# Optimization experiments

Hardware: AMD Instinct MI355X
Metric: run time of the kernel (lower is better)

The kernel has to match this reference:

```python
import jax, jax.numpy as jnp
import numpy as np

N_NODES = 100000
N_EDGES = 1600000
K = 3  # TAGConv default hops


def _make_lin(key, out_dim, in_dim):
    # K+1 bias-free linears (stacked) + one shared output bias, per PyG TAGConv
    kw, = jax.random.split(key, 1)
    scale = 1.0 / np.sqrt(in_dim)
    W = jax.random.uniform(kw, (K + 1, out_dim, in_dim), jnp.float32, -scale, scale)
    b = jnp.zeros((out_dim,), jnp.float32)
    return W, b


def setup_inputs() -> dict:
    key = jax.random.key(0)
    ks = jax.random.split(key, 6)
    x = jax.random.normal(ks[0], (N_NODES, 128), jnp.float32)
    edge_index = jax.random.randint(ks[1], (2, N_EDGES), 0, N_NODES, jnp.int64)
    W1, b1 = _make_lin(ks[2], 128, 128)
    W2, b2 = _make_lin(ks[3], 64, 128)
    W3, b3 = _make_lin(ks[4], 16, 64)
    return {"x": x, "edge_index": edge_index, "W1": W1, "b1": b1,
            "W2": W2, "b2": b2, "W3": W3, "b3": b3}


def _tagconv(x, row, col, norm, W, b, n):
    # out = sum_k lin_k(A_norm^k x) + b ; message x_j*norm gathered at col
    out = jnp.einsum('nd,od->no', x, W[0])
    h = x
    for k in range(1, W.shape[0]):
        h = jax.ops.segment_sum(norm[:, None] * h[row], col, num_segments=n)
        out = out + jnp.einsum('nd,od->no', h, W[k])
    return out + b


def _dropout(x, key, p=0.5):
    keep = jax.random.bernoulli(key, 1.0 - p, x.shape)
    return jnp.where(keep, x / (1.0 - p), 0.0)


def reference(x, edge_index, W1, b1, W2, b2, W3, b3):
    n = x.shape[0]
    row, col = edge_index[0], edge_index[1]
    # gcn_norm without self-loops (TAGConv default)
    deg = jax.ops.segment_sum(jnp.ones(row.shape[0], x.dtype), col, num_segments=n)
    dis = jnp.where(deg > 0, 1.0 / jnp.sqrt(jnp.where(deg > 0, deg, 1.0)), 0.0)
    norm = dis[row] * dis[col]

    dk1, dk2 = jax.random.split(jax.random.key(42))
    h = _tagconv(x, row, col, norm, W1, b1, n)
    h = _dropout(h, dk1)
    h = _tagconv(h, row, col, norm, W2, b2, n)
    h = jax.nn.elu(h)
    h = _dropout(h, dk2)
    h = _tagconv(h, row, col, norm, W3, b3, n)
    return h
```

## Files before the change

### kernel.cpp

```cpp
#include <hip/hip_runtime.h>
#include <stdint.h>
#include <math.h>

#define N_NODES 100000
#define N_EDGES 1600000

typedef __bf16 bf16_t;
typedef __attribute__((ext_vector_type(4))) __bf16 bf16x4;
typedef __attribute__((ext_vector_type(8))) __bf16 bf16x8;
typedef __attribute__((ext_vector_type(4))) float f32x4;

__device__ __forceinline__ f32x4 mfma16(bf16x8 a, bf16x8 b, f32x4 c) {
  return __builtin_amdgcn_mfma_f32_16x16x32_bf16(a, b, c, 0, 0, 0);
}

__device__ __host__ __forceinline__ uint32_t rotl32(uint32_t v, int d) {
  return (v << d) | (v >> (32 - d));
}

__device__ __host__ __forceinline__ void threefry2x32(uint32_t k0, uint32_t k1,
                                                      uint32_t x0, uint32_t x1,
                                                      uint32_t& o0, uint32_t& o1) {
  uint32_t ks0 = k0, ks1 = k1, ks2 = k0 ^ k1 ^ 0x1BD11BDAu;
  x0 += ks0; x1 += ks1;
#define TF_R(r) { x0 += x1; x1 = rotl32(x1, r); x1 ^= x0; }
  TF_R(13) TF_R(15) TF_R(26) TF_R(6)
  x0 += ks1; x1 += ks2 + 1u;
  TF_R(17) TF_R(29) TF_R(16) TF_R(24)
  x0 += ks2; x1 += ks0 + 2u;
  TF_R(13) TF_R(15) TF_R(26) TF_R(6)
  x0 += ks0; x1 += ks1 + 3u;
  TF_R(17) TF_R(29) TF_R(16) TF_R(24)
  x0 += ks1; x1 += ks2 + 4u;
  TF_R(13) TF_R(15) TF_R(26) TF_R(6)
  x0 += ks2; x1 += ks0 + 5u;
#undef TF_R
  o0 = x0; o1 = x1;
}

__device__ __forceinline__ float drop_scale(uint32_t idx, uint32_t k0, uint32_t k1) {
  uint32_t o0, o1;
  threefry2x32(k0, k1, 0u, idx, o0, o1);
  uint32_t bits = o0 ^ o1;
  float u = __uint_as_float((bits >> 9) | 0x3f800000u) - 1.0f;
  return (u < 0.5f) ? 2.0f : 0.0f;
}

__global__ __launch_bounds__(256) void detect_kernel(const int* __restrict__ ei,
                                                     int* __restrict__ found_nonzero) {
  int idx = blockIdx.x * 256 + threadIdx.x;
  size_t j = (size_t)idx * 781;
  if (ei[2 * j + 1] != 0) atomicOr(found_nonzero, 1);
}

__device__ __forceinline__ int edge_row(const int* ei, bool i32, int e) {
  return i32 ? ei[e] : ei[2 * (size_t)e];
}
__device__ __forceinline__ int edge_col(const int* ei, bool i32, int e) {
  return i32 ? ei[N_EDGES + e] : ei[2 * ((size_t)N_EDGES + (size_t)e)];
}

#define BKT_SHIFT 8
#define NBKT 391
#define BKT_CAP 6144
#define EPB 8192
#define NBLK 196
#define SCAN_M (NBKT * NBLK)

__global__ __launch_bounds__(256) void hist_kernel(const int* __restrict__ ei,
                                                   const int* __restrict__ flag,
                                                   int* __restrict__ hist) {
  __shared__ int h[NBKT];
  const int t = threadIdx.x, blk = blockIdx.x;
  for (int i = t; i < NBKT; i += 256) h[i] = 0;
  __syncthreads();
  const bool i32 = *flag != 0;
  const int e0 = blk * EPB;
  for (int i = t; i < EPB; i += 256) {
    int e = e0 + i;
    if (e < N_EDGES) atomicAdd(&h[edge_col(ei, i32, e) >> BKT_SHIFT], 1);
  }
  __syncthreads();
  for (int i = t; i < NBKT; i += 256) hist[i * NBLK + blk] = h[i];
}

__global__ __launch_bounds__(256) void btot_kernel(const int* __restrict__ hist,
                                                   int* __restrict__ btot) {
  __shared__ int sh[256];
  const int b = blockIdx.x, t = threadIdx.x;
  int s = 0;
  for (int i = t; i < NBLK; i += 256) s += hist[b * NBLK + i];
  sh[t] = s;
  __syncthreads();
  for (int ofs = 128; ofs > 0; ofs >>= 1) {
    if (t < ofs) sh[t] += sh[t + ofs];
    __syncthreads();
  }
  if (t == 0) btot[b] = sh[0];
}

__global__ __launch_bounds__(512) void bbase_kernel(const int* __restrict__ btot,
                                                    int* __restrict__ bbase,
                                                    int* __restrict__ S) {
  __shared__ int sh[512];
  const int t = threadIdx.x;
  int v = (t < NBKT) ? btot[t] : 0;
  sh[t] = v;
  __syncthreads();
  for (int ofs = 1; ofs < 512; ofs <<= 1) {
    int u = (t >= ofs) ? sh[t - ofs] : 0;
    __syncthreads();
    sh[t] += u;
    __syncthreads();
  }
  if (t < NBKT) bbase[t] = sh[t] - v;
  if (t == 0) S[SCAN_M] = N_EDGES;
}

__global__ __launch_bounds__(256) void bscan2_kernel(const int* __restrict__ hist,
                                                     const int* __restrict__ bbase,
                                                     int* __restrict__ S) {
  __shared__ int sh[256];
  const int b = blockIdx.x, t = threadIdx.x;
  int v = (t < NBLK) ? hist[b * NBLK + t] : 0;
  sh[t] = v;
  __syncthreads();
  for (int ofs = 1; ofs < 256; ofs <<= 1) {
    int u = (t >= ofs) ? sh[t - ofs] : 0;
    __syncthreads();
    sh[t] += u;
    __syncthreads();
  }
  if (t < NBLK) S[b * NBLK + t] = bbase[b] + sh[t] - v;
}

__global__ __launch_bounds__(256) void binfill_kernel(const int* __restrict__ ei,
                                                      const int* __restrict__ flag,
                                                      const int* __restrict__ S,
                                                      int2* __restrict__ bins) {
  __shared__ int cur[NBKT];
  const int t = threadIdx.x, blk = blockIdx.x;
  for (int i = t; i < NBKT; i += 256) cur[i] = S[i * NBLK + blk];
  __syncthreads();
  const bool i32 = *flag != 0;
  const int e0 = blk * EPB;
  for (int i = t; i < EPB; i += 256) {
    int e = e0 + i;
    if (e < N_EDGES) {
      int r = edge_row(ei, i32, e);
      int c = edge_col(ei, i32, e);
      int p = atomicAdd(&cur[c >> BKT_SHIFT], 1);
      bins[p] = make_int2(r, c);
    }
  }
}

__global__ __launch_bounds__(512) void degdis_scatter_kernel(
    const int2* __restrict__ bins, const int* __restrict__ S,
    float* __restrict__ dis, int* __restrict__ rptr,
    uint32_t* __restrict__ erow) {
  __shared__ int h[256];
  __shared__ int sc[256];
  __shared__ int loff[256];
  __shared__ int lcur[256];
  __shared__ uint32_t reord[BKT_CAP];
  const int b = blockIdx.x, t = threadIdx.x;
  const int Bb = S[b * NBLK];
  const int Be = S[(b + 1) * NBLK];
  const int cnt = min(Be - Bb, BKT_CAP);
  if (t < 256) h[t] = 0;
  __syncthreads();
  for (int i = t; i < cnt; i += 512)
    atomicAdd(&h[bins[Bb + i].y & 255], 1);
  __syncthreads();
  if (t < 256) sc[t] = h[t];
  __syncthreads();
  for (int ofs = 1; ofs < 256; ofs <<= 1) {
    int u = 0;
    if (t >= ofs && t < 256) u = sc[t - ofs];
    __syncthreads();
    if (t < 256) sc[t] += u;
    __syncthreads();
  }
  const int c0 = b << BKT_SHIFT;
  const int nn = min(256, N_NODES - c0);
  if (t < 256) {
    loff[t] = sc[t] - h[t];
    lcur[t] = 0;
    if (t < nn) {
      int d = h[t];
      dis[c0 + t] = (d > 0) ? (1.0f / sqrtf((float)d)) : 0.0f;
      rptr[c0 + t] = Bb + sc[t] - d;
    }
  }
  if (b == NBKT - 1 && t == 0) rptr[N_NODES] = N_EDGES;
  __syncthreads();
  for (int i = t; i < cnt; i += 512) {
    int2 rec = bins[Bb + i];
    int lc = rec.y & 255;
    int p = atomicAdd(&lcur[lc], 1);
    reord[loff[lc] + p] = (uint32_t)rec.x;
  }
  __syncthreads();
  for (int i = t; i < cnt; i += 512) erow[Bb + i] = reord[i];
}

__global__ __launch_bounds__(256) void wcvt_kernel(
    const float* __restrict__ W1, const float* __restrict__ W2,
    const float* __restrict__ W3,
    bf16_t* __restrict__ Wb1, bf16_t* __restrict__ Wb2,
    bf16_t* __restrict__ Wb3) {
  int i = blockIdx.x * 256 + threadIdx.x;
  if (i < 65536) Wb1[i] = (bf16_t)W1[i];
  if (i < 32768) Wb2[i] = (bf16_t)W2[i];
  if (i < 4096)  Wb3[i] = (bf16_t)W3[i];
}

template <int DIN, int LOG_DOUT, int NCH, bool YB, bool AHL>
__global__ __launch_bounds__(256) void matmul_mfma_kernel(
    const void* __restrict__ hA, const void* __restrict__ hAlo,
    const bf16_t* __restrict__ Wb, const float* __restrict__ bias,
    float* __restrict__ y0, void* __restrict__ y1,
    void* __restrict__ y2, void* __restrict__ y3) {
  constexpr int LDK = DIN + 8;
  constexpr int DOUT = 1 << LOG_DOUT;
  constexpr int KI = DIN / 32;
  __shared__ bf16_t sm[2][64 * LDK];
  const int m0 = blockIdx.x * 64;
  const int tid = threadIdx.x;

  if (AHL) {
    constexpr int NL = 64 * DIN / 8 / 256;
#pragma unroll
    for (int it = 0; it < NL; ++it) {
      int idx = tid + it * 256;
      int r = idx / (DIN / 8), cc = (idx % (DIN / 8)) * 8;
      int gm = m0 + r;
      uint4 vh = make_uint4(0, 0, 0, 0), vl = make_uint4(0, 0, 0, 0);
      if (gm < N_NODES) {
        vh = ((const uint4*)hA)[((size_t)gm * DIN + cc) >> 3];
        vl = ((const uint4*)hAlo)[((size_t)gm * DIN + cc) >> 3];
      }
      *(uint4*)&sm[0][r * LDK + cc] = vh;
      *(uint4*)&sm[1][r * LDK + cc] = vl;
    }
  } else {
    constexpr int NL = 64 * DIN / 4 / 256;
    union U4 { bf16_t b[4]; uint2 u; };
#pragma unroll
    for (int it = 0; it < NL; ++it) {
      int idx = tid + it * 256;
      int r = idx / (DIN / 4), cc = (idx % (DIN / 4)) * 4;
      int gm = m0 + r;
      float4 v = (gm < N_NODES) ? ((const float4*)hA)[((size_t)gm * DIN + cc) >> 2]
                                : make_float4(0.f, 0.f, 0.f, 0.f);
      U4 hi, lo;
      hi.b[0] = (bf16_t)v.x; lo.b[0] = (bf16_t)(v.x - (float)hi.b[0]);
      hi.b[1] = (bf16_t)v.y; lo.b[1] = (bf16_t)(v.y - (float)hi.b[1]);
      hi.b[2] = (bf16_t)v.z; lo.b[2] = (bf16_t)(v.z - (float)hi.b[2]);
      hi.b[3] = (bf16_t)v.w; lo.b[3] = (bf16_t)(v.w - (float)hi.b[3]);
      *(uint2*)&sm[0][r * LDK + cc] = hi.u;
      *(uint2*)&sm[1][r * LDK + cc] = lo.u;
    }
  }
  __syncthreads();

  const int w = tid >> 6, lane = tid & 63;
  const int wm = w & 1, wn = w >> 1;
  const int quad = lane >> 4, lr = lane & 15;

  bf16x8 aH[2][KI], aL[2][KI];
#pragma unroll
  for (int mt = 0; mt < 2; ++mt)
#pragma unroll
    for (int ki = 0; ki < KI; ++ki) {
      int rowa = wm * 32 + mt * 16 + lr;
      int koff = ki * 32 + quad * 8;
      aH[mt][ki] = *(const bf16x8*)&sm[0][rowa * LDK + koff];
      aL[mt][ki] = *(const bf16x8*)&sm[1][rowa * LDK + koff];
    }
  __syncthreads();

  constexpr int NLB = 64 * DIN / 8 / 256;
  uint4 wreg[NLB];
#pragma unroll
  for (int it = 0; it < NLB; ++it) {
    int idx = tid + it * 256;
    int r = idx / (DIN / 8), cc = (idx % (DIN / 8)) * 8;
    wreg[it] = ((const uint4*)Wb)[(((size_t)r) * DIN + cc) >> 3];
    *(uint4*)&sm[0][r * LDK + cc] = wreg[it];
  }
  __syncthreads();

  for (int nc = 0; nc < NCH; ++nc) {
    int p = nc & 1;
    if (nc + 1 < NCH) {
#pragma unroll
      for (int it = 0; it < NLB; ++it) {
        int idx = tid + it * 256;
        int r = idx / (DIN / 8), cc = (idx % (DIN / 8)) * 8;
        wreg[it] = ((const uint4*)Wb)[(((size_t)((nc + 1) * 64 + r)) * DIN + cc) >> 3];
      }
    }

    f32x4 acc[2][2] = {};
#pragma unroll
    for (int ki = 0; ki < KI; ++ki) {
      int koff = ki * 32 + quad * 8;
      bf16x8 bfr[2];
#pragma unroll
      for (int nt = 0; nt < 2; ++nt)
        bfr[nt] = *(const bf16x8*)&sm[p][(wn * 32 + nt * 16 + lr) * LDK + koff];
#pragma unroll
      for (int mt = 0; mt < 2; ++mt)
#pragma unroll
        for (int nt = 0; nt < 2; ++nt) {
          acc[mt][nt] = mfma16(bfr[nt], aH[mt][ki], acc[mt][nt]);
          acc[mt][nt] = mfma16(bfr[nt], aL[mt][ki], acc[mt][nt]);
        }
    }

    if (nc + 1 < NCH) {
#pragma unroll
      for (int it = 0; it < NLB; ++it) {
        int idx = tid + it * 256;
        int r = idx / (DIN / 8), cc = (idx % (DIN / 8)) * 8;
        *(uint4*)&sm[p ^ 1][r * LDK + cc] = wreg[it];
      }
    }
    __syncthreads();

    const int n0 = nc * 64;
#pragma unroll
    for (int mt = 0; mt < 2; ++mt) {
      int m = m0 + wm * 32 + mt * 16 + lr;
      if (m >= N_NODES) continue;
#pragma unroll
      for (int nt = 0; nt < 2; ++nt) {
        int nb = n0 + wn * 32 + nt * 16 + quad * 4;
        int k = nb >> LOG_DOUT;
        int o = nb & (DOUT - 1);
        size_t oi = (size_t)m * DOUT + o;
        if (k == 0) {
          float4 bv = *(const float4*)&bias[o];
          float4 st = make_float4(acc[mt][nt][0] + bv.x, acc[mt][nt][1] + bv.y,
                                  acc[mt][nt][2] + bv.z, acc[mt][nt][3] + bv.w);
          *(float4*)&y0[oi] = st;
        } else {
          void* yk = (k == 1) ? y1 : (k == 2) ? y2 : y3;
          if (YB) {
            bf16x4 bb;
            bb.x = (bf16_t)acc[mt][nt][0];
            bb.y = (bf16_t)acc[mt][nt][1];
            bb.z = (bf16_t)acc[mt][nt][2];
            bb.w = (bf16_t)acc[mt][nt][3];
            *(bf16x4*)((bf16_t*)yk + oi) = bb;
          } else {
            *(f32x4*)((float*)yk + oi) = acc[mt][nt];
          }
        }
      }
    }
  }
}

template <int D, int EPI, bool ABF, int OMODE>
__global__ __launch_bounds__(256) void prop_kernel(
    const bf16_t* __restrict__ zv, const void* __restrict__ addv,
    void* __restrict__ outv, void* __restrict__ outv2,
    const int* __restrict__ rptr, const uint32_t* __restrict__ erow,
    const float* __restrict__ dis, uint32_t k0, uint32_t k1) {
  constexpr int LPN = D / 4;
  constexpr int NPB = 256 / LPN;
  const int lane = threadIdx.x % LPN;
  const int nsub = threadIdx.x / LPN;
  const int c = blockIdx.x * NPB + nsub;
  if (c >= N_NODES) return;
  const int e0 = rptr[c], e1 = rptr[c + 1];
  const float dc = dis[c];
  const bf16x4* zs = (const bf16x4*)zv;
  float a0 = 0.f, a1 = 0.f, a2 = 0.f, a3 = 0.f;

  int e = e0;
  for (; e + 7 < e1; e += 8) {
    uint32_t r8[8];
#pragma unroll
    for (int j = 0; j < 8; ++j) r8[j] = erow[e + j];
    float w8[8];
    bf16x4 v8[8];
#pragma unroll
    for (int j = 0; j < 8; ++j) {
      w8[j] = dis[r8[j]];
      v8[j] = zs[(size_t)r8[j] * LPN + lane];
    }
#pragma unroll
    for (int j = 0; j < 8; ++j) {
      float w = w8[j] * dc;
      a0 = fmaf(w, (float)v8[j].x, a0);
      a1 = fmaf(w, (float)v8[j].y, a1);
      a2 = fmaf(w, (float)v8[j].z, a2);
      a3 = fmaf(w, (float)v8[j].w, a3);
    }
  }
  if (e + 3 < e1) {
    uint32_t r4[4];
#pragma unroll
    for (int j = 0; j < 4; ++j) r4[j] = erow[e + j];
    float w4[4];
    bf16x4 v4[4];
#pragma unroll
    for (int j = 0; j < 4; ++j) {
      w4[j] = dis[r4[j]];
      v4[j] = zs[(size_t)r4[j] * LPN + lane];
    }
#pragma unroll
    for (int j = 0; j < 4; ++j) {
      float w = w4[j] * dc;
      a0 = fmaf(w, (float)v4[j].x, a0);
      a1 = fmaf(w, (float)v4[j].y, a1);
      a2 = fmaf(w, (float)v4[j].z, a2);
      a3 = fmaf(w, (float)v4[j].w, a3);
    }
    e += 4;
  }
  for (; e < e1; ++e) {
    uint32_t r = erow[e];
    float w = dis[r] * dc;
    bf16x4 t = zs[(size_t)r * LPN + lane];
    a0 = fmaf(w, (float)t.x, a0);
    a1 = fmaf(w, (float)t.y, a1);
    a2 = fmaf(w, (float)t.z, a2);
    a3 = fmaf(w, (float)t.w, a3);
  }

  const size_t pidx = (size_t)c * LPN + lane;
  const uint32_t fidx = (uint32_t)c * D + 4 * lane;
  float ax[4];
  if (ABF) {
    bf16x4 t = ((const bf16x4*)addv)[pidx];
    ax[0] = (float)t.x; ax[1] = (float)t.y; ax[2] = (float)t.z; ax[3] = (float)t.w;
  } else {
    float4 t = ((const float4*)addv)[pidx];
    ax[0] = t.x; ax[1] = t.y; ax[2] = t.z; ax[3] = t.w;
  }
  float o[4] = {a0 + ax[0], a1 + ax[1], a2 + ax[2], a3 + ax[3]};
  if (EPI == 1) {
#pragma unroll
    for (int j = 0; j < 4; ++j) o[j] *= drop_scale(fidx + j, k0, k1);
  }
  if (EPI == 2) {
#pragma unroll
    for (int j = 0; j < 4; ++j) {
      o[j] = (o[j] > 0.f) ? o[j] : expm1f(o[j]);
      o[j] *= drop_scale(fidx + j, k0, k1);
    }
  }
  if (OMODE == 0) {
    ((float4*)outv)[pidx] = make_float4(o[0], o[1], o[2], o[3]);
  } else if (OMODE == 1) {
    bf16x4 bv;
    bv.x = (bf16_t)o[0]; bv.y = (bf16_t)o[1];
    bv.z = (bf16_t)o[2]; bv.w = (bf16_t)o[3];
    ((bf16x4*)outv)[pidx] = bv;
  } else {
    bf16x4 hv, lv;
    hv.x = (bf16_t)o[0]; hv.y = (bf16_t)o[1];
    hv.z = (bf16_t)o[2]; hv.w = (bf16_t)o[3];
    lv.x = (bf16_t)(o[0] - (float)hv.x);
    lv.y = (bf16_t)(o[1] - (float)hv.y);
    lv.z = (bf16_t)(o[2] - (float)hv.z);
    lv.w = (bf16_t)(o[3] - (float)hv.w);
    ((bf16x4*)outv)[pidx] = hv;
    ((bf16x4*)outv2)[pidx] = lv;
  }
}

extern "C" void kernel_launch(void* const* d_in, const int* in_sizes, int n_in,
                              void* d_out, int out_size, void* d_ws, size_t ws_size,
                              hipStream_t stream) {
  const float* x  = (const float*)d_in[0];
  const int*   ei = (const int*)d_in[1];
  const float* W1 = (const float*)d_in[2];
  const float* b1 = (const float*)d_in[3];
  const float* W2 = (const float*)d_in[4];
  const float* b2 = (const float*)d_in[5];
  const float* W3 = (const float*)d_in[6];
  const float* b3 = (const float*)d_in[7];
  float* out = (float*)d_out;

  char* ws = (char*)d_ws;
  size_t off = 0;
  auto alloc = [&](size_t bytes) -> char* {
    char* p = ws + off;
    off += (bytes + 255) & ~(size_t)255;
    return p;
  };
  int*   flag   = (int*)alloc(256);
  float* dis    = (float*)alloc((size_t)N_NODES * 4);
  int*   rptr   = (int*)alloc((size_t)(N_NODES + 1) * 4);
  int*   hist   = (int*)alloc((size_t)SCAN_M * 4);
  int*   S      = (int*)alloc((size_t)(SCAN_M + 1) * 4);
  int*   btot   = (int*)alloc((size_t)NBKT * 4);
  int*   bbase  = (int*)alloc((size_t)NBKT * 4);
  uint32_t* erow = (uint32_t*)alloc((size_t)N_EDGES * 4);
  bf16_t* Wb1  = (bf16_t*)alloc(65536 * 2);
  bf16_t* Wb2  = (bf16_t*)alloc(32768 * 2);
  bf16_t* Wb3  = (bf16_t*)alloc(4096 * 2);
  float*  R0  = (float*)alloc((size_t)N_NODES * 128 * 4);
  float*  R2  = (float*)alloc((size_t)N_NODES * 16 * 4);
  bf16_t* Zb0 = (bf16_t*)alloc((size_t)N_NODES * 128 * 2);
  bf16_t* Zb1 = (bf16_t*)alloc((size_t)N_NODES * 128 * 2);
  bf16_t* Bb1 = (bf16_t*)alloc((size_t)N_NODES * 128 * 2);
  bf16_t* Bb2 = (bf16_t*)alloc((size_t)N_NODES * 128 * 2);

  int2* bins = (int2*)R0;

  hipMemsetAsync(flag, 0, 256, stream);

  detect_kernel<<<8, 256, 0, stream>>>(ei, flag);
  hist_kernel<<<NBLK, 256, 0, stream>>>(ei, flag, hist);
  btot_kernel<<<NBKT, 256, 0, stream>>>(hist, btot);
  bbase_kernel<<<1, 512, 0, stream>>>(btot, bbase, S);
  bscan2_kernel<<<NBKT, 256, 0, stream>>>(hist, bbase, S);
  binfill_kernel<<<NBLK, 256, 0, stream>>>(ei, flag, S, bins);
  degdis_scatter_kernel<<<NBKT, 512, 0, stream>>>(bins, S, dis, rptr, erow);
  wcvt_kernel<<<256, 256, 0, stream>>>(W1, W2, W3, Wb1, Wb2, Wb3);

  uint32_t d10, d11, d20, d21;
  threefry2x32(0u, 42u, 0u, 0u, d10, d11);
  threefry2x32(0u, 42u, 0u, 1u, d20, d21);

  const int MB = (N_NODES + 63) / 64;
  const int PB128 = (N_NODES + 7) / 8;
  const int PB64n = (N_NODES + 15) / 16;
  const int PB16n = (N_NODES + 63) / 64;

  matmul_mfma_kernel<128, 7, 8, true, false><<<MB, 256, 0, stream>>>(
      x, nullptr, Wb1, b1, R0, Bb1, Bb2, Zb0);
  prop_kernel<128, 0, true, 1><<<PB128, 256, 0, stream>>>(
      Zb0, Bb2, Zb1, nullptr, rptr, erow, dis, 0, 0);
  prop_kernel<128, 0, true, 1><<<PB128, 256, 0, stream>>>(
      Zb1, Bb1, Zb0, nullptr, rptr, erow, dis, 0, 0);
  prop_kernel<128, 1, false, 2><<<PB128, 256, 0, stream>>>(
      Zb0, R0, Bb2, Bb1, rptr, erow, dis, d10, d11);

  float*  R1f = R0;
  bf16_t* S0 = Zb0;
  bf16_t* S1 = Zb0 + (size_t)N_NODES * 64;
  bf16_t* S2 = Zb1;
  bf16_t* S3 = Zb1 + (size_t)N_NODES * 64;
  matmul_mfma_kernel<128, 6, 4, true, true><<<MB, 256, 0, stream>>>(
      Bb2, Bb1, Wb2, b2, R1f, S2, S3, S0);
  prop_kernel<64, 0, true, 1><<<PB64n, 256, 0, stream>>>(
      S0, S3, S1, nullptr, rptr, erow, dis, 0, 0);
  prop_kernel<64, 0, true, 1><<<PB64n, 256, 0, stream>>>(
      S1, S2, S0, nullptr, rptr, erow, dis, 0, 0);
  prop_kernel<64, 2, false, 2><<<PB64n, 256, 0, stream>>>(
      S0, R1f, S2, S3, rptr, erow, dis, d20, d21);

  float*  z0f = R2;
  bf16_t* zb1 = Bb1;
  bf16_t* zb2 = Bb1 + (size_t)N_NODES * 16;
  bf16_t* zb3 = Bb1 + (size_t)N_NODES * 32;
  matmul_mfma_kernel<64, 4, 1, true, true><<<MB, 256, 0, stream>>>(
      S2, S3, Wb3, b3, z0f, zb1, zb2, zb3);
  prop_kernel<16, 0, true, 1><<<PB16n, 256, 0, stream>>>(
      zb3, zb2, zb2, nullptr, rptr, erow, dis, 0, 0);
  prop_kernel<16, 0, true, 1><<<PB16n, 256, 0, stream>>>(
      zb2, zb1, zb1, nullptr, rptr, erow, dis, 0, 0);
  prop_kernel<16, 0, false, 0><<<PB16n, 256, 0, stream>>>(
      zb1, z0f, out, nullptr, rptr, erow, dis, 0, 0);

  (void)in_sizes; (void)n_in; (void)out_size; (void)ws_size;
}
```

Measured before the change: 647.1 us.

## Load MFMA operands directly from global memory, dropping LDS staging

```diff
diff --git a/kernel.cpp b/kernel.cpp
--- a/kernel.cpp
+++ b/kernel.cpp
@@ -222,113 +222,68 @@
     const bf16_t* __restrict__ Wb, const float* __restrict__ bias,
     float* __restrict__ y0, void* __restrict__ y1,
     void* __restrict__ y2, void* __restrict__ y3) {
-  constexpr int LDK = DIN + 8;
   constexpr int DOUT = 1 << LOG_DOUT;
   constexpr int KI = DIN / 32;
-  __shared__ bf16_t sm[2][64 * LDK];
   const int m0 = blockIdx.x * 64;
   const int tid = threadIdx.x;
-
-  if (AHL) {
-    constexpr int NL = 64 * DIN / 8 / 256;
-#pragma unroll
-    for (int it = 0; it < NL; ++it) {
-      int idx = tid + it * 256;
-      int r = idx / (DIN / 8), cc = (idx % (DIN / 8)) * 8;
-      int gm = m0 + r;
-      uint4 vh = make_uint4(0, 0, 0, 0), vl = make_uint4(0, 0, 0, 0);
-      if (gm < N_NODES) {
-        vh = ((const uint4*)hA)[((size_t)gm * DIN + cc) >> 3];
-        vl = ((const uint4*)hAlo)[((size_t)gm * DIN + cc) >> 3];
-      }
-      *(uint4*)&sm[0][r * LDK + cc] = vh;
-      *(uint4*)&sm[1][r * LDK + cc] = vl;
-    }
-  } else {
-    constexpr int NL = 64 * DIN / 4 / 256;
-    union U4 { bf16_t b[4]; uint2 u; };
-#pragma unroll
-    for (int it = 0; it < NL; ++it) {
-      int idx = tid + it * 256;
-      int r = idx / (DIN / 4), cc = (idx % (DIN / 4)) * 4;
-      int gm = m0 + r;
-      float4 v = (gm < N_NODES) ? ((const float4*)hA)[((size_t)gm * DIN + cc) >> 2]
-                                : make_float4(0.f, 0.f, 0.f, 0.f);
-      U4 hi, lo;
-      hi.b[0] = (bf16_t)v.x; lo.b[0] = (bf16_t)(v.x - (float)hi.b[0]);
-      hi.b[1] = (bf16_t)v.y; lo.b[1] = (bf16_t)(v.y - (float)hi.b[1]);
-      hi.b[2] = (bf16_t)v.z; lo.b[2] = (bf16_t)(v.z - (float)hi.b[2]);
-      hi.b[3] = (bf16_t)v.w; lo.b[3] = (bf16_t)(v.w - (float)hi.b[3]);
-      *(uint2*)&sm[0][r * LDK + cc] = hi.u;
-      *(uint2*)&sm[1][r * LDK + cc] = lo.u;
-    }
-  }
-  __syncthreads();
-
   const int w = tid >> 6, lane = tid & 63;
   const int wm = w & 1, wn = w >> 1;
   const int quad = lane >> 4, lr = lane & 15;
 
   bf16x8 aH[2][KI], aL[2][KI];
 #pragma unroll
-  for (int mt = 0; mt < 2; ++mt)
+  for (int mt = 0; mt < 2; ++mt) {
+    const int gm = m0 + wm * 32 + mt * 16 + lr;
+    const bool ok = gm < N_NODES;
 #pragma unroll
     for (int ki = 0; ki < KI; ++ki) {
-      int rowa = wm * 32 + mt * 16 + lr;
-      int koff = ki * 32 + quad * 8;
-      aH[mt][ki] = *(const bf16x8*)&sm[0][rowa * LDK + koff];
-      aL[mt][ki] = *(const bf16x8*)&sm[1][rowa * LDK + koff];
-    }
-  __syncthreads();
-
-  constexpr int NLB = 64 * DIN / 8 / 256;
-  uint4 wreg[NLB];
-#pragma unroll
-  for (int it = 0; it < NLB; ++it) {
-    int idx = tid + it * 256;
-    int r = idx / (DIN / 8), cc = (idx % (DIN / 8)) * 8;
-    wreg[it] = ((const uint4*)Wb)[(((size_t)r) * DIN + cc) >> 3];
-    *(uint4*)&sm[0][r * LDK + cc] = wreg[it];
-  }
-  __syncthreads();
+      const int koff = ki * 32 + quad * 8;
+      if (AHL) {
+        if (ok) {
+          aH[mt][ki] = *(const bf16x8*)((const bf16_t*)hA + (size_t)gm * DIN + koff);
+          aL[mt][ki] = *(const bf16x8*)((const bf16_t*)hAlo + (size_t)gm * DIN + koff);
+        } else {
+#pragma unroll
+          for (int q = 0; q < 8; ++q) { aH[mt][ki][q] = (bf16_t)0.f; aL[mt][ki][q] = (bf16_t)0.f; }
+        }
+      } else {
+        float4 v0 = make_float4(0.f, 0.f, 0.f, 0.f), v1 = v0;
+        if (ok) {
+          const float* xp = (const float*)hA + (size_t)gm * DIN + koff;
+          v0 = *(const float4*)xp;
+          v1 = *(const float4*)(xp + 4);
+        }
+        float vv[8] = {v0.x, v0.y, v0.z, v0.w, v1.x, v1.y, v1.z, v1.w};
+#pragma unroll
+        for (int q = 0; q < 8; ++q) {
+          bf16_t hi = (bf16_t)vv[q];
+          aH[mt][ki][q] = hi;
+          aL[mt][ki][q] = (bf16_t)(vv[q] - (float)hi);
+        }
+      }
+    }
+  }
 
   for (int nc = 0; nc < NCH; ++nc) {
-    int p = nc & 1;
-    if (nc + 1 < NCH) {
-#pragma unroll
-      for (int it = 0; it < NLB; ++it) {
-        int idx = tid + it * 256;
-        int r = idx / (DIN / 8), cc = (idx % (DIN / 8)) * 8;
-        wreg[it] = ((const uint4*)Wb)[(((size_t)((nc + 1) * 64 + r)) * DIN + cc) >> 3];
-      }
+    bf16x8 bfr[2][KI];
+#pragma unroll
+    for (int nt = 0; nt < 2; ++nt) {
+      const int wr = nc * 64 + wn * 32 + nt * 16 + lr;
+#pragma unroll
+      for (int ki = 0; ki < KI; ++ki)
+        bfr[nt][ki] = *(const bf16x8*)&Wb[(size_t)wr * DIN + ki * 32 + quad * 8];
     }
 
     f32x4 acc[2][2] = {};
 #pragma unroll
-    for (int ki = 0; ki < KI; ++ki) {
-      int koff = ki * 32 + quad * 8;
-      bf16x8 bfr[2];
-#pragma unroll
-      for (int nt = 0; nt < 2; ++nt)
-        bfr[nt] = *(const bf16x8*)&sm[p][(wn * 32 + nt * 16 + lr) * LDK + koff];
+    for (int ki = 0; ki < KI; ++ki)
 #pragma unroll
       for (int mt = 0; mt < 2; ++mt)
 #pragma unroll
         for (int nt = 0; nt < 2; ++nt) {
-          acc[mt][nt] = mfma16(bfr[nt], aH[mt][ki], acc[mt][nt]);
-          acc[mt][nt] = mfma16(bfr[nt], aL[mt][ki], acc[mt][nt]);
+          acc[mt][nt] = mfma16(bfr[nt][ki], aH[mt][ki], acc[mt][nt]);
+          acc[mt][nt] = mfma16(bfr[nt][ki], aL[mt][ki], acc[mt][nt]);
         }
-    }
-
-    if (nc + 1 < NCH) {
-#pragma unroll
-      for (int it = 0; it < NLB; ++it) {
-        int idx = tid + it * 256;
-        int r = idx / (DIN / 8), cc = (idx % (DIN / 8)) * 8;
-        *(uint4*)&sm[p ^ 1][r * LDK + cc] = wreg[it];
-      }
-    }
-    __syncthreads();
 
     const int n0 = nc * 64;
 #pragma unroll
```

Result: slower. 677.6 us (+4.7%).
